# Optimization experiments

Measured on AMD Instinct MI355X. Metric: run time of the kernel, lower is better.

The kernel has to match this reference:

```python
import jax, jax.numpy as jnp
import numpy as np

B, N, C, H, D = 1, 4096, 256, 8, 64  # batch, seq, channels, heads, head_dim


def setup_inputs() -> dict:
    key = jax.random.key(0)
    ks = jax.random.split(key, 11)
    s = 0.02
    return {
        "q_x": jax.random.normal(ks[0], (B, N, C), jnp.float32),
        "k_x": jax.random.normal(ks[1], (B, N, C), jnp.float32),
        "v_x": jax.random.normal(ks[2], (B, N, C), jnp.float32),
        "bias": jax.random.normal(ks[3], (B, 1, N, N), jnp.float32),
        "wq": jax.random.normal(ks[4], (H * D, C), jnp.float32) * s,
        "wk": jax.random.normal(ks[5], (H * D, C), jnp.float32) * s,
        "wv": jax.random.normal(ks[6], (H * D, C), jnp.float32) * s,
        "wg": jax.random.normal(ks[7], (H * D, C), jnp.float32) * s,
        "bg": jnp.ones((H * D,), jnp.float32),  # gating bias init = 1
        "wo": jax.random.normal(ks[8], (C, H * D), jnp.float32) * s,
        "bo": jnp.zeros((C,), jnp.float32),
        "q_chunk_size": 256,
        "kv_chunk_size": 1024,
    }


def reference(q_x, k_x, v_x, bias, wq, wk, wv, wg, bg, wo, bo,
              q_chunk_size, kv_chunk_size):
    # The chunked Rabe-Staats loop computes exact softmax attention; the
    # chunk sizes are memory knobs only, so the reference computes the
    # mathematically identical full attention.
    q = (q_x @ wq.T).reshape(*q_x.shape[:-1], H, D) / jnp.sqrt(jnp.asarray(D, q_x.dtype))
    k = (k_x @ wk.T).reshape(*k_x.shape[:-1], H, D)
    v = (v_x @ wv.T).reshape(*v_x.shape[:-1], H, D)
    logits = jnp.einsum("bqhd,bkhd->bhqk", q, k) + bias  # [B,H,Q,K]
    p = jax.nn.softmax(logits, axis=-1)
    o = jnp.einsum("bkhd,bhqk->bqhd", v, p)  # [B,Q,H,D]
    g = jax.nn.sigmoid(q_x @ wg.T + bg).reshape(*q_x.shape[:-1], H, D)
    o = o * g
    o = o.reshape(*o.shape[:-2], H * D)
    return o @ wo.T + bo
```

## Files before the change

### kernel.cpp

```cpp
#include <hip/hip_runtime.h>
#include <stdint.h>

#define NN 4096
#define CC 256
#define HD 512
#define DD 64
#define KSPLIT 3
#define KSPLIT_O 4

typedef __attribute__((ext_vector_type(8))) short short8;
typedef __attribute__((ext_vector_type(4))) float floatx4;

__device__ __forceinline__ unsigned short f2bf(float x) {
    union { float f; unsigned int u; } v; v.f = x;
    unsigned int u = v.u + 0x7fffu + ((v.u >> 16) & 1u);
    return (unsigned short)(u >> 16);
}
__device__ __forceinline__ float bf2f(unsigned short s) {
    union { unsigned int u; float f; } v; v.u = ((unsigned int)s) << 16;
    return v.f;
}

#if defined(__has_builtin) && __has_builtin(__builtin_amdgcn_cvt_pk_bf16_f32)
typedef __attribute__((ext_vector_type(2))) __bf16 bf16x2_t;
__device__ __forceinline__ unsigned int pack2bf(float a, float b) {
    union { bf16x2_t v; unsigned int u; } x;
    x.v = __builtin_amdgcn_cvt_pk_bf16_f32(a, b);
    return x.u;
}
#else
__device__ __forceinline__ unsigned int pack2bf(float a, float b) {
    return ((unsigned int)f2bf(b) << 16) | (unsigned int)f2bf(a);
}
#endif

#define GLOAD_LDS(gp, lp) __builtin_amdgcn_global_load_lds(                    \
    (__attribute__((address_space(1))) void*)(gp),                             \
    (__attribute__((address_space(3))) void*)(lp), 16, 0, 0)

__global__ __launch_bounds__(256) void prep_kernel(
    const float* __restrict__ qx, const float* __restrict__ kx,
    const float* __restrict__ vx,
    const float* __restrict__ wq, const float* __restrict__ wk,
    const float* __restrict__ wv, const float* __restrict__ wg,
    const float* __restrict__ wo,
    unsigned short* __restrict__ qxb, unsigned short* __restrict__ kxb,
    unsigned short* __restrict__ vxb, unsigned short* __restrict__ Wb,
    unsigned short* __restrict__ wob)
{
    const int z = blockIdx.y;
    const float* src; unsigned short* dst; int n; float s = 1.0f;
    switch (z) {
        case 0: src = qx; dst = qxb; n = NN * CC; break;
        case 1: src = kx; dst = kxb; n = NN * CC; break;
        case 2: src = vx; dst = vxb; n = NN * CC; break;
        case 3: src = wq; dst = Wb;               n = HD * CC; s = 0.125f; break;
        case 4: src = wk; dst = Wb + 1 * HD * CC; n = HD * CC; break;
        case 5: src = wv; dst = Wb + 2 * HD * CC; n = HD * CC; break;
        case 6: src = wg; dst = Wb + 3 * HD * CC; n = HD * CC; break;
        default: src = wo; dst = wob;             n = CC * HD; break;
    }
    int i = (blockIdx.x * 256 + threadIdx.x) * 4;
    if (i < n) {
        float4 v = *(const float4*)&src[i];
        ushort4 p;
        p.x = f2bf(v.x * s); p.y = f2bf(v.y * s);
        p.z = f2bf(v.z * s); p.w = f2bf(v.w * s);
        *(ushort4*)&dst[i] = p;
    }
}

__global__ __launch_bounds__(256, 4) void proj_kernel(
    const unsigned short* __restrict__ qxb, const unsigned short* __restrict__ kxb,
    const unsigned short* __restrict__ vxb, const unsigned short* __restrict__ Wb,
    const float* __restrict__ bg,
    unsigned short* __restrict__ Qb, unsigned short* __restrict__ Kb,
    unsigned short* __restrict__ VbT, unsigned short* __restrict__ Gb)
{
    const int m0 = blockIdx.x * 64;
    const int nb = blockIdx.y;
    const int n0 = nb * 128;
    const int mode = nb >> 2;
    const unsigned short* X = (mode == 1) ? kxb : (mode == 2) ? vxb : qxb;

    const int tid = threadIdx.x;
    const int wid = tid >> 6;
    const int lane = tid & 63;
    const int quad = lane >> 4;
    const int ln = lane & 15;
    const int lnx = ln & 7;

    __shared__ __align__(16) unsigned short smem[64 * 64 + 128 * 64];
    unsigned short* Xs = smem;
    unsigned short* Ws = smem + 64 * 64;

    floatx4 acc[8] = {};

    for (int k0 = 0; k0 < CC; k0 += 64) {
        #pragma unroll
        for (int t = 0; t < 2; t++) {
            int row = wid * 16 + t * 8 + (lane >> 3);
            int c = (lane & 7) ^ (lane >> 3);
            GLOAD_LDS(&X[(size_t)(m0 + row) * CC + k0 + c * 8],
                      &Xs[(wid * 16 + t * 8) * 64]);
        }
        #pragma unroll
        for (int t = 0; t < 4; t++) {
            int row = wid * 32 + t * 8 + (lane >> 3);
            int c = (lane & 7) ^ (lane >> 3);
            GLOAD_LDS(&Wb[(size_t)(n0 + row) * CC + k0 + c * 8],
                      &Ws[(wid * 32 + t * 8) * 64]);
        }
        __syncthreads();

        #pragma unroll
        for (int ks = 0; ks < 64; ks += 32) {
            const int cb = ks >> 3;
            short8 a = *(const short8*)&Xs[(wid * 16 + ln) * 64 +
                                           (((quad ^ cb) ^ lnx) * 8)];
            #pragma unroll
            for (int j = 0; j < 8; j++) {
                short8 b = *(const short8*)&Ws[(j * 16 + ln) * 64 +
                                               (((quad ^ cb) ^ lnx) * 8)];
                acc[j] = __builtin_amdgcn_mfma_f32_16x16x32_bf16(a, b, acc[j], 0, 0, 0);
            }
        }
        __syncthreads();
    }

    const int subn = nb & 3;
    if (mode != 2) {
        unsigned short* Out = (mode == 0) ? Qb : (mode == 1) ? Kb : Gb;
        #pragma unroll
        for (int j = 0; j < 8; j++) {
            int col = subn * 128 + j * 16 + ln;
            float bgv = (mode == 3) ? bg[col] : 0.0f;
            #pragma unroll
            for (int r = 0; r < 4; r++) {
                int row = m0 + wid * 16 + quad * 4 + r;
                float v = acc[j][r];
                if (mode == 3) v = 1.0f / (1.0f + __expf(-(v + bgv)));
                Out[(size_t)row * HD + col] = f2bf(v);
            }
        }
    } else {
        #pragma unroll
        for (int j = 0; j < 8; j++) {
            int cl = j * 16 + ln;
            #pragma unroll
            for (int r = 0; r < 4; r++) {
                int rl = wid * 16 + quad * 4 + r;
                smem[cl * 72 + rl] = f2bf(acc[j][r]);
            }
        }
        __syncthreads();
        #pragma unroll
        for (int it = 0; it < 4; it++) {
            int idx = it * 256 + tid;
            int c = idx >> 3, ch = idx & 7;
            short8 vv = *(const short8*)&smem[c * 72 + ch * 8];
            *(short8*)&VbT[(size_t)(subn * 128 + c) * NN + m0 + ch * 8] = vv;
        }
    }
}

__global__ __launch_bounds__(256, 6) void attn_kernel(
    const unsigned short* __restrict__ Qb, const unsigned short* __restrict__ Kb,
    const unsigned short* __restrict__ VbT,
    const float* __restrict__ bias,
    unsigned short* __restrict__ Opart, float* __restrict__ Lpart)
{
    const int h = blockIdx.y;
    const int q0 = blockIdx.x * 64;
    const int sp = blockIdx.z;
    const int tbeg = (sp * 64) / KSPLIT;
    const int tend = ((sp + 1) * 64) / KSPLIT;
    const int tid = threadIdx.x;
    const int wid = tid >> 6;
    const int lane = tid & 63;
    const int quad = lane >> 4;
    const int ln = lane & 15;
    const int lnx = ln & 7;

    __shared__ __align__(16) unsigned short Ks[64 * 64];
    __shared__ __align__(16) unsigned short Vs[64 * 64];
    __shared__ __align__(16) unsigned short Ps[64 * 72];

    const int qrow = q0 + wid * 16 + ln;
    short8 qa0 = *(const short8*)&Qb[(size_t)qrow * HD + h * DD + quad * 8];
    short8 qa1 = *(const short8*)&Qb[(size_t)qrow * HD + h * DD + 32 + quad * 8];

    floatx4 O[4] = {};
    float lsum[4] = {0.0f, 0.0f, 0.0f, 0.0f};

    for (int kt = tbeg; kt < tend; kt++) {
        const int k0 = kt * 64;
        #pragma unroll
        for (int t = 0; t < 2; t++) {
            int row = wid * 16 + t * 8 + (lane >> 3);
            int c = (lane & 7) ^ (lane >> 3);
            GLOAD_LDS(&Kb[(size_t)(k0 + row) * HD + h * DD + c * 8],
                      &Ks[(wid * 16 + t * 8) * 64]);
            GLOAD_LDS(&VbT[(size_t)(h * DD + row) * NN + k0 + c * 8],
                      &Vs[(wid * 16 + t * 8) * 64]);
        }

        float bv[4][4];
        #pragma unroll
        for (int r = 0; r < 4; r++) {
            const float* brow = &bias[(size_t)(q0 + wid * 16 + quad * 4 + r) * NN + k0];
            #pragma unroll
            for (int n = 0; n < 4; n++) bv[r][n] = brow[n * 16 + ln];
        }
        __syncthreads();

        floatx4 S[4];
        #pragma unroll
        for (int n = 0; n < 4; n++)
            S[n] = (floatx4){bv[0][n], bv[1][n], bv[2][n], bv[3][n]};
        #pragma unroll
        for (int n = 0; n < 4; n++) {
            short8 b0 = *(const short8*)&Ks[(n * 16 + ln) * 64 + ((quad ^ lnx) * 8)];
            S[n] = __builtin_amdgcn_mfma_f32_16x16x32_bf16(qa0, b0, S[n], 0, 0, 0);
            short8 b1 = *(const short8*)&Ks[(n * 16 + ln) * 64 + (((quad ^ 4) ^ lnx) * 8)];
            S[n] = __builtin_amdgcn_mfma_f32_16x16x32_bf16(qa1, b1, S[n], 0, 0, 0);
        }

        #pragma unroll
        for (int r = 0; r < 4; r++) {
            int prow = (wid * 16 + quad * 4 + r) * 72;
            #pragma unroll
            for (int n = 0; n < 4; n += 2) {
                float p0 = __expf(S[n][r]);
                float p1 = __expf(S[n + 1][r]);
                lsum[r] += p0 + p1;
                unsigned int pk = pack2bf(p0, p1);
                Ps[prow + n * 16 + ln] = (unsigned short)(pk & 0xffffu);
                Ps[prow + (n + 1) * 16 + ln] = (unsigned short)(pk >> 16);
            }
        }

        #pragma unroll
        for (int ks = 0; ks < 64; ks += 32) {
            const int cb = ks >> 3;
            short8 a = *(const short8*)&Ps[(wid * 16 + ln) * 72 + ks + quad * 8];
            #pragma unroll
            for (int nd = 0; nd < 4; nd++) {
                short8 b = *(const short8*)&Vs[(nd * 16 + ln) * 64 +
                                               (((quad ^ cb) ^ lnx) * 8)];
                O[nd] = __builtin_amdgcn_mfma_f32_16x16x32_bf16(a, b, O[nd], 0, 0, 0);
            }
        }
        __syncthreads();
    }

    #pragma unroll
    for (int r = 0; r < 4; r++) {
        #pragma unroll
        for (int off = 1; off < 16; off <<= 1)
            lsum[r] += __shfl_xor(lsum[r], off);
        int grow = q0 + wid * 16 + quad * 4 + r;
        size_t base = ((size_t)(sp * 8 + h) * NN + grow) * 64;
        #pragma unroll
        for (int nd = 0; nd < 4; nd++)
            Opart[base + nd * 16 + ln] = f2bf(O[nd][r]);
        if (ln == 0)
            Lpart[(size_t)(sp * 8 + h) * NN + grow] = lsum[r];
    }
}

__global__ __launch_bounds__(256) void combine_kernel(
    const unsigned short* __restrict__ Opart, const float* __restrict__ Lpart,
    const unsigned short* __restrict__ Gb, unsigned short* __restrict__ OGb)
{
    const int tid = threadIdx.x;
    const int d = tid & 63;
    const int flat = blockIdx.x * 4 + (tid >> 6);
    const int h = flat >> 12;
    const int q = flat & (NN - 1);

    float l = 0.0f, o = 0.0f;
    #pragma unroll
    for (int sp = 0; sp < KSPLIT; sp++) {
        size_t idx = (size_t)(sp * 8 + h) * NN + q;
        l += Lpart[idx];
        o += bf2f(Opart[idx * 64 + d]);
    }
    float inv = 1.0f / l;
    int col = h * DD + d;
    float g = bf2f(Gb[(size_t)q * HD + col]);
    OGb[(size_t)q * HD + col] = f2bf(o * inv * g);
}

__global__ __launch_bounds__(256, 4) void outproj_kernel(
    const unsigned short* __restrict__ OGb, const unsigned short* __restrict__ wob,
    float* __restrict__ Psum)
{
    const int m0 = blockIdx.x * 64;
    const int n0 = blockIdx.y * 64;
    const int sp = blockIdx.z;
    const int tid = threadIdx.x;
    const int wid = tid >> 6;
    const int lane = tid & 63;
    const int quad = lane >> 4;
    const int ln = lane & 15;
    const int lnx = ln & 7;

    __shared__ __align__(16) unsigned short Xs[64 * 64];
    __shared__ __align__(16) unsigned short Ws[64 * 64];

    floatx4 acc[4] = {};

    const int kbeg = sp * (HD / KSPLIT_O);
    for (int k0 = kbeg; k0 < kbeg + HD / KSPLIT_O; k0 += 64) {
        #pragma unroll
        for (int t = 0; t < 2; t++) {
            int row = wid * 16 + t * 8 + (lane >> 3);
            int c = (lane & 7) ^ (lane >> 3);
            GLOAD_LDS(&OGb[(size_t)(m0 + row) * HD + k0 + c * 8],
                      &Xs[(wid * 16 + t * 8) * 64]);
            GLOAD_LDS(&wob[(size_t)(n0 + row) * HD + k0 + c * 8],
                      &Ws[(wid * 16 + t * 8) * 64]);
        }
        __syncthreads();

        #pragma unroll
        for (int ks = 0; ks < 64; ks += 32) {
            const int cb = ks >> 3;
            short8 a = *(const short8*)&Xs[(wid * 16 + ln) * 64 +
                                           (((quad ^ cb) ^ lnx) * 8)];
            #pragma unroll
            for (int n = 0; n < 4; n++) {
                short8 b = *(const short8*)&Ws[(n * 16 + ln) * 64 +
                                               (((quad ^ cb) ^ lnx) * 8)];
                acc[n] = __builtin_amdgcn_mfma_f32_16x16x32_bf16(a, b, acc[n], 0, 0, 0);
            }
        }
        __syncthreads();
    }

    float* P = Psum + (size_t)sp * NN * CC;
    #pragma unroll
    for (int n = 0; n < 4; n++) {
        int col = n0 + n * 16 + ln;
        #pragma unroll
        for (int r = 0; r < 4; r++) {
            int row = m0 + wid * 16 + quad * 4 + r;
            P[(size_t)row * CC + col] = acc[n][r];
        }
    }
}

__global__ __launch_bounds__(256) void outfinal_kernel(
    const float* __restrict__ Psum, const float* __restrict__ bo,
    float* __restrict__ out)
{
    int i = (blockIdx.x * 256 + threadIdx.x) * 4;
    float4 s = *(const float4*)&Psum[i];
    #pragma unroll
    for (int sp = 1; sp < KSPLIT_O; sp++) {
        float4 p = *(const float4*)&Psum[(size_t)sp * NN * CC + i];
        s.x += p.x; s.y += p.y; s.z += p.z; s.w += p.w;
    }
    int col = i & (CC - 1);
    float4 b = *(const float4*)&bo[col];
    s.x += b.x; s.y += b.y; s.z += b.z; s.w += b.w;
    *(float4*)&out[i] = s;
}

extern "C" void kernel_launch(void* const* d_in, const int* in_sizes, int n_in,
                              void* d_out, int out_size, void* d_ws, size_t ws_size,
                              hipStream_t stream) {
    const float* qx   = (const float*)d_in[0];
    const float* kx   = (const float*)d_in[1];
    const float* vx   = (const float*)d_in[2];
    const float* bias = (const float*)d_in[3];
    const float* wq   = (const float*)d_in[4];
    const float* wk   = (const float*)d_in[5];
    const float* wv   = (const float*)d_in[6];
    const float* wg   = (const float*)d_in[7];
    const float* bg   = (const float*)d_in[8];
    const float* wo   = (const float*)d_in[9];
    const float* bo   = (const float*)d_in[10];
    float* out = (float*)d_out;

    char* ws = (char*)d_ws;
    const size_t MB = (size_t)1 << 20;
    unsigned short* wob   = (unsigned short*)(ws);
    float*          Lpart = (float*)(ws + MB / 4);
    unsigned short* Qb    = (unsigned short*)(ws + 1 * MB);
    unsigned short* Kb    = (unsigned short*)(ws + 5 * MB);
    unsigned short* VbT   = (unsigned short*)(ws + 9 * MB);
    unsigned short* Gb    = (unsigned short*)(ws + 13 * MB);
    unsigned short* OGb   = (unsigned short*)(ws + 17 * MB);
    unsigned short* qxb   = (unsigned short*)(ws + 21 * MB);
    unsigned short* kxb   = (unsigned short*)(ws + 23 * MB);
    unsigned short* vxb   = (unsigned short*)(ws + 25 * MB);
    unsigned short* Wb    = (unsigned short*)(ws + 27 * MB);
    unsigned short* Opart = (unsigned short*)(ws + 21 * MB);
    float*          Psum  = (float*)(ws + 21 * MB);

    prep_kernel<<<dim3(NN * CC / (256 * 4), 8), 256, 0, stream>>>(
        qx, kx, vx, wq, wk, wv, wg, wo, qxb, kxb, vxb, Wb, wob);
    proj_kernel<<<dim3(64, 16), 256, 0, stream>>>(
        qxb, kxb, vxb, Wb, bg, Qb, Kb, VbT, Gb);
    attn_kernel<<<dim3(64, 8, KSPLIT), 256, 0, stream>>>(
        Qb, Kb, VbT, bias, Opart, Lpart);
    combine_kernel<<<dim3(NN * 8 / 4), 256, 0, stream>>>(
        Opart, Lpart, Gb, OGb);
    outproj_kernel<<<dim3(64, 4, KSPLIT_O), 256, 0, stream>>>(
        OGb, wob, Psum);
    outfinal_kernel<<<dim3(NN * CC / (256 * 4)), 256, 0, stream>>>(
        Psum, bo, out);
}
```

Before: 220.0 us.

## Fuse split-K combine into attention via atomic last-block and drop outproj split

The separate combine kernel is removed. Each attention block now bumps an atomic counter for its (head, query tile), and the last of the KSPLIT blocks to finish reduces the partial outputs, applies the gate and writes OGb. The output projection loses its K-split: it accumulates the full HD dimension and adds the bias directly, which removes the Psum buffer and the outfinal kernel. Counters are zeroed in an extra prep_kernel slice. This cuts two launches and the partial-sum round trips through memory, but adds a serial tail to the last attention blocks and leaves the out-projection grid four times smaller.

After: 532.0 us. 2.42x slower.

```diff
diff --git a/kernel.cpp b/kernel.cpp
--- a/kernel.cpp
+++ b/kernel.cpp
@@ -6,7 +6,6 @@
 #define HD 512
 #define DD 64
 #define KSPLIT 3
-#define KSPLIT_O 4
 
 typedef __attribute__((ext_vector_type(8))) short short8;
 typedef __attribute__((ext_vector_type(4))) float floatx4;
@@ -46,9 +45,16 @@
     const float* __restrict__ wo,
     unsigned short* __restrict__ qxb, unsigned short* __restrict__ kxb,
     unsigned short* __restrict__ vxb, unsigned short* __restrict__ Wb,
-    unsigned short* __restrict__ wob)
+    unsigned short* __restrict__ wob, int* __restrict__ counters)
 {
     const int z = blockIdx.y;
+    if (z == 8) {
+        if (blockIdx.x == 0) {
+            counters[threadIdx.x] = 0;
+            counters[256 + threadIdx.x] = 0;
+        }
+        return;
+    }
     const float* src; unsigned short* dst; int n; float s = 1.0f;
     switch (z) {
         case 0: src = qx; dst = qxb; n = NN * CC; break;
@@ -168,7 +174,8 @@
     const unsigned short* __restrict__ Qb, const unsigned short* __restrict__ Kb,
     const unsigned short* __restrict__ VbT,
     const float* __restrict__ bias,
-    unsigned short* __restrict__ Opart, float* __restrict__ Lpart)
+    unsigned short* Opart, float* Lpart, int* counters,
+    const unsigned short* __restrict__ Gb, unsigned short* __restrict__ OGb)
 {
     const int h = blockIdx.y;
     const int q0 = blockIdx.x * 64;
@@ -185,6 +192,7 @@
     __shared__ __align__(16) unsigned short Ks[64 * 64];
     __shared__ __align__(16) unsigned short Vs[64 * 64];
     __shared__ __align__(16) unsigned short Ps[64 * 72];
+    __shared__ int s_last;
 
     const int qrow = q0 + wid * 16 + ln;
     short8 qa0 = *(const short8*)&Qb[(size_t)qrow * HD + h * DD + quad * 8];
@@ -267,38 +275,42 @@
         if (ln == 0)
             Lpart[(size_t)(sp * 8 + h) * NN + grow] = lsum[r];
     }
-}
-
-__global__ __launch_bounds__(256) void combine_kernel(
-    const unsigned short* __restrict__ Opart, const float* __restrict__ Lpart,
-    const unsigned short* __restrict__ Gb, unsigned short* __restrict__ OGb)
-{
-    const int tid = threadIdx.x;
-    const int d = tid & 63;
-    const int flat = blockIdx.x * 4 + (tid >> 6);
-    const int h = flat >> 12;
-    const int q = flat & (NN - 1);
-
-    float l = 0.0f, o = 0.0f;
-    #pragma unroll
-    for (int sp = 0; sp < KSPLIT; sp++) {
-        size_t idx = (size_t)(sp * 8 + h) * NN + q;
-        l += Lpart[idx];
-        o += bf2f(Opart[idx * 64 + d]);
-    }
-    float inv = 1.0f / l;
-    int col = h * DD + d;
-    float g = bf2f(Gb[(size_t)q * HD + col]);
-    OGb[(size_t)q * HD + col] = f2bf(o * inv * g);
+
+    __threadfence();
+    __syncthreads();
+    if (tid == 0) {
+        int old = __hip_atomic_fetch_add(&counters[h * 64 + blockIdx.x], 1,
+                                         __ATOMIC_ACQ_REL, __HIP_MEMORY_SCOPE_AGENT);
+        s_last = (old == KSPLIT - 1);
+    }
+    __syncthreads();
+    if (s_last) {
+        __threadfence();
+        const int d = tid & 63;
+        const int rg = tid >> 6;
+        #pragma unroll
+        for (int rr = 0; rr < 16; rr++) {
+            int q = q0 + rg * 16 + rr;
+            float l = 0.0f, o = 0.0f;
+            #pragma unroll
+            for (int s2 = 0; s2 < KSPLIT; s2++) {
+                size_t idx = (size_t)(s2 * 8 + h) * NN + q;
+                l += Lpart[idx];
+                o += bf2f(Opart[idx * 64 + d]);
+            }
+            int col = h * DD + d;
+            float g = bf2f(Gb[(size_t)q * HD + col]);
+            OGb[(size_t)q * HD + col] = f2bf(o / l * g);
+        }
+    }
 }
 
 __global__ __launch_bounds__(256, 4) void outproj_kernel(
     const unsigned short* __restrict__ OGb, const unsigned short* __restrict__ wob,
-    float* __restrict__ Psum)
+    const float* __restrict__ bo, float* __restrict__ out)
 {
     const int m0 = blockIdx.x * 64;
     const int n0 = blockIdx.y * 64;
-    const int sp = blockIdx.z;
     const int tid = threadIdx.x;
     const int wid = tid >> 6;
     const int lane = tid & 63;
@@ -311,8 +323,7 @@
 
     floatx4 acc[4] = {};
 
-    const int kbeg = sp * (HD / KSPLIT_O);
-    for (int k0 = kbeg; k0 < kbeg + HD / KSPLIT_O; k0 += 64) {
+    for (int k0 = 0; k0 < HD; k0 += 64) {
         #pragma unroll
         for (int t = 0; t < 2; t++) {
             int row = wid * 16 + t * 8 + (lane >> 3);
@@ -339,33 +350,16 @@
         __syncthreads();
     }
 
-    float* P = Psum + (size_t)sp * NN * CC;
     #pragma unroll
     for (int n = 0; n < 4; n++) {
         int col = n0 + n * 16 + ln;
+        float bov = bo[col];
         #pragma unroll
         for (int r = 0; r < 4; r++) {
             int row = m0 + wid * 16 + quad * 4 + r;
-            P[(size_t)row * CC + col] = acc[n][r];
-        }
-    }
-}
-
-__global__ __launch_bounds__(256) void outfinal_kernel(
-    const float* __restrict__ Psum, const float* __restrict__ bo,
-    float* __restrict__ out)
-{
-    int i = (blockIdx.x * 256 + threadIdx.x) * 4;
-    float4 s = *(const float4*)&Psum[i];
-    #pragma unroll
-    for (int sp = 1; sp < KSPLIT_O; sp++) {
-        float4 p = *(const float4*)&Psum[(size_t)sp * NN * CC + i];
-        s.x += p.x; s.y += p.y; s.z += p.z; s.w += p.w;
-    }
-    int col = i & (CC - 1);
-    float4 b = *(const float4*)&bo[col];
-    s.x += b.x; s.y += b.y; s.z += b.z; s.w += b.w;
-    *(float4*)&out[i] = s;
+            out[(size_t)row * CC + col] = acc[n][r] + bov;
+        }
+    }
 }
 
 extern "C" void kernel_launch(void* const* d_in, const int* in_sizes, int n_in,
@@ -386,8 +380,9 @@
 
     char* ws = (char*)d_ws;
     const size_t MB = (size_t)1 << 20;
-    unsigned short* wob   = (unsigned short*)(ws);
-    float*          Lpart = (float*)(ws + MB / 4);
+    unsigned short* wob      = (unsigned short*)(ws);
+    float*          Lpart    = (float*)(ws + MB / 4);
+    int*            counters = (int*)(ws + MB / 2 + MB / 4);
     unsigned short* Qb    = (unsigned short*)(ws + 1 * MB);
     unsigned short* Kb    = (unsigned short*)(ws + 5 * MB);
     unsigned short* VbT   = (unsigned short*)(ws + 9 * MB);
@@ -398,18 +393,13 @@
     unsigned short* vxb   = (unsigned short*)(ws + 25 * MB);
     unsigned short* Wb    = (unsigned short*)(ws + 27 * MB);
     unsigned short* Opart = (unsigned short*)(ws + 21 * MB);
-    float*          Psum  = (float*)(ws + 21 * MB);
-
-    prep_kernel<<<dim3(NN * CC / (256 * 4), 8), 256, 0, stream>>>(
-        qx, kx, vx, wq, wk, wv, wg, wo, qxb, kxb, vxb, Wb, wob);
+
+    prep_kernel<<<dim3(NN * CC / (256 * 4), 9), 256, 0, stream>>>(
+        qx, kx, vx, wq, wk, wv, wg, wo, qxb, kxb, vxb, Wb, wob, counters);
     proj_kernel<<<dim3(64, 16), 256, 0, stream>>>(
         qxb, kxb, vxb, Wb, bg, Qb, Kb, VbT, Gb);
     attn_kernel<<<dim3(64, 8, KSPLIT), 256, 0, stream>>>(
-        Qb, Kb, VbT, bias, Opart, Lpart);
-    combine_kernel<<<dim3(NN * 8 / 4), 256, 0, stream>>>(
-        Opart, Lpart, Gb, OGb);
-    outproj_kernel<<<dim3(64, 4, KSPLIT_O), 256, 0, stream>>>(
-        OGb, wob, Psum);
-    outfinal_kernel<<<dim3(NN * CC / (256 * 4)), 256, 0, stream>>>(
-        Psum, bo, out);
-}
+        Qb, Kb, VbT, bias, Opart, Lpart, counters, Gb, OGb);
+    outproj_kernel<<<dim3(64, 4), 256, 0, stream>>>(
+        OGb, wob, bo, out);
+}
```

## Prefetch next bias tile in attention and drop split-K from output projection

Applied to the files above, without the earlier changes.

The attention kernel now loads the next kv tile's bias values into registers during the current tile's compute, so global bias latency overlaps the MFMA work instead of stalling before the first barrier. The output projection no longer splits K four ways into partial sums. It accumulates over the full 512 width and writes the final output with bias directly, which removes the Psum round trip and the separate reduction kernel launch. The trade-offs are higher register pressure in attention and fewer output-projection blocks, 256 instead of 1024, each doing a longer loop.

Result: slower. 271.5 us (+23.5%).

```diff
diff --git a/kernel.cpp b/kernel.cpp
--- a/kernel.cpp
+++ b/kernel.cpp
@@ -6,7 +6,6 @@
 #define HD 512
 #define DD 64
 #define KSPLIT 3
-#define KSPLIT_O 4
 
 typedef __attribute__((ext_vector_type(8))) short short8;
 typedef __attribute__((ext_vector_type(4))) float floatx4;
@@ -190,8 +189,23 @@
     short8 qa0 = *(const short8*)&Qb[(size_t)qrow * HD + h * DD + quad * 8];
     short8 qa1 = *(const short8*)&Qb[(size_t)qrow * HD + h * DD + 32 + quad * 8];
 
+    const float* bias_row[4];
+    #pragma unroll
+    for (int r = 0; r < 4; r++)
+        bias_row[r] = &bias[(size_t)(q0 + wid * 16 + quad * 4 + r) * NN + ln];
+
     floatx4 O[4] = {};
     float lsum[4] = {0.0f, 0.0f, 0.0f, 0.0f};
+
+    float bv[4][4];
+    {
+        const int k0 = tbeg * 64;
+        #pragma unroll
+        for (int r = 0; r < 4; r++)
+            #pragma unroll
+            for (int n = 0; n < 4; n++)
+                bv[r][n] = bias_row[r][k0 + n * 16];
+    }
 
     for (int kt = tbeg; kt < tend; kt++) {
         const int k0 = kt * 64;
@@ -204,15 +218,17 @@
             GLOAD_LDS(&VbT[(size_t)(h * DD + row) * NN + k0 + c * 8],
                       &Vs[(wid * 16 + t * 8) * 64]);
         }
-
-        float bv[4][4];
-        #pragma unroll
-        for (int r = 0; r < 4; r++) {
-            const float* brow = &bias[(size_t)(q0 + wid * 16 + quad * 4 + r) * NN + k0];
-            #pragma unroll
-            for (int n = 0; n < 4; n++) bv[r][n] = brow[n * 16 + ln];
-        }
-        __syncthreads();
+        __syncthreads();
+
+        float bvn[4][4];
+        if (kt + 1 < tend) {
+            const int k1 = (kt + 1) * 64;
+            #pragma unroll
+            for (int r = 0; r < 4; r++)
+                #pragma unroll
+                for (int n = 0; n < 4; n++)
+                    bvn[r][n] = bias_row[r][k1 + n * 16];
+        }
 
         floatx4 S[4];
         #pragma unroll
@@ -252,6 +268,14 @@
             }
         }
         __syncthreads();
+
+        if (kt + 1 < tend) {
+            #pragma unroll
+            for (int r = 0; r < 4; r++)
+                #pragma unroll
+                for (int n = 0; n < 4; n++)
+                    bv[r][n] = bvn[r][n];
+        }
     }
 
     #pragma unroll
@@ -294,11 +318,10 @@
 
 __global__ __launch_bounds__(256, 4) void outproj_kernel(
     const unsigned short* __restrict__ OGb, const unsigned short* __restrict__ wob,
-    float* __restrict__ Psum)
+    const float* __restrict__ bo, float* __restrict__ out)
 {
     const int m0 = blockIdx.x * 64;
     const int n0 = blockIdx.y * 64;
-    const int sp = blockIdx.z;
     const int tid = threadIdx.x;
     const int wid = tid >> 6;
     const int lane = tid & 63;
@@ -311,8 +334,7 @@
 
     floatx4 acc[4] = {};
 
-    const int kbeg = sp * (HD / KSPLIT_O);
-    for (int k0 = kbeg; k0 < kbeg + HD / KSPLIT_O; k0 += 64) {
+    for (int k0 = 0; k0 < HD; k0 += 64) {
         #pragma unroll
         for (int t = 0; t < 2; t++) {
             int row = wid * 16 + t * 8 + (lane >> 3);
@@ -339,33 +361,16 @@
         __syncthreads();
     }
 
-    float* P = Psum + (size_t)sp * NN * CC;
     #pragma unroll
     for (int n = 0; n < 4; n++) {
         int col = n0 + n * 16 + ln;
+        float bov = bo[col];
         #pragma unroll
         for (int r = 0; r < 4; r++) {
             int row = m0 + wid * 16 + quad * 4 + r;
-            P[(size_t)row * CC + col] = acc[n][r];
-        }
-    }
-}
-
-__global__ __launch_bounds__(256) void outfinal_kernel(
-    const float* __restrict__ Psum, const float* __restrict__ bo,
-    float* __restrict__ out)
-{
-    int i = (blockIdx.x * 256 + threadIdx.x) * 4;
-    float4 s = *(const float4*)&Psum[i];
-    #pragma unroll
-    for (int sp = 1; sp < KSPLIT_O; sp++) {
-        float4 p = *(const float4*)&Psum[(size_t)sp * NN * CC + i];
-        s.x += p.x; s.y += p.y; s.z += p.z; s.w += p.w;
-    }
-    int col = i & (CC - 1);
-    float4 b = *(const float4*)&bo[col];
-    s.x += b.x; s.y += b.y; s.z += b.z; s.w += b.w;
-    *(float4*)&out[i] = s;
+            out[(size_t)row * CC + col] = acc[n][r] + bov;
+        }
+    }
 }
 
 extern "C" void kernel_launch(void* const* d_in, const int* in_sizes, int n_in,
@@ -398,7 +403,6 @@
     unsigned short* vxb   = (unsigned short*)(ws + 25 * MB);
     unsigned short* Wb    = (unsigned short*)(ws + 27 * MB);
     unsigned short* Opart = (unsigned short*)(ws + 21 * MB);
-    float*          Psum  = (float*)(ws + 21 * MB);
 
     prep_kernel<<<dim3(NN * CC / (256 * 4), 8), 256, 0, stream>>>(
         qx, kx, vx, wq, wk, wv, wg, wo, qxb, kxb, vxb, Wb, wob);
@@ -408,8 +412,6 @@
         Qb, Kb, VbT, bias, Opart, Lpart);
     combine_kernel<<<dim3(NN * 8 / 4), 256, 0, stream>>>(
         Opart, Lpart, Gb, OGb);
-    outproj_kernel<<<dim3(64, 4, KSPLIT_O), 256, 0, stream>>>(
-        OGb, wob, Psum);
-    outfinal_kernel<<<dim3(NN * CC / (256 * 4)), 256, 0, stream>>>(
-        Psum, bo, out);
-}
+    outproj_kernel<<<dim3(64, 4), 256, 0, stream>>>(
+        OGb, wob, bo, out);
+}
```
